# Kernel optimization log

Hardware: AMD Instinct MI355X
Metric: run time of the kernel (lower is better)

## Reference

```python
import jax, jax.numpy as jnp
import numpy as np

HD_DIM = 4096
BUNDLE_SIZE = 128
STRIDE = 128  # bundle_size - overlap, overlap = 0
EPS = 1e-8


def setup_inputs() -> dict:
    key = jax.random.key(0)
    k1, k2 = jax.random.split(key)
    inputs = jax.random.normal(k1, (4, 2048, HD_DIM), dtype=jnp.float32)
    # base vector ~ N(0, 1/sqrt(hd_dim)) as in RandomNormal(stddev=1/sqrt(hd_dim))
    base = jax.random.normal(k2, (HD_DIM,), dtype=jnp.float32) / jnp.sqrt(jnp.float32(HD_DIM))
    # position_weights initialized to decay_rate**i
    pos_w = jnp.power(jnp.float32(0.99), jnp.arange(BUNDLE_SIZE, dtype=jnp.float32))
    return {"inputs": inputs, "bundle_position_base": base, "position_weights": pos_w}


def reference(inputs, bundle_position_base, position_weights):
    B, S, D = inputs.shape
    nb = (S - BUNDLE_SIZE) // STRIDE + 1  # number of bundles

    # Cyclic-shift position vectors: pos[s, d] = base[(d - s) mod D]
    shifts = jnp.arange(BUNDLE_SIZE)
    idx = jnp.mod(jnp.arange(D)[None, :] - shifts[:, None], D)  # [bs, D]
    pos = bundle_position_base[idx]                              # [bs, D]
    w = jax.nn.softmax(position_weights)                         # [bs]
    pos = pos * w[:, None]

    # overlap=0 and S divisible by bundle_size -> bundles tile the sequence
    tok = inputs.reshape(B, nb, BUNDLE_SIZE, D)  # [B, nb, bs, D]

    # circular correlation: real(ifft(fft(tok) * conj(fft(pos))))
    # both operands real -> use rfft/irfft (identical math, half the work)
    tok_f = jnp.fft.rfft(tok, axis=-1)                 # [B, nb, bs, D//2+1]
    pos_f = jnp.conj(jnp.fft.rfft(pos, axis=-1))       # [bs, D//2+1]
    bound = jnp.fft.irfft(tok_f * pos_f[None, None], n=D, axis=-1)  # [B, nb, bs, D]

    bundle = jnp.sum(bound, axis=2)  # [B, nb, D]
    # tf.nn.l2_normalize: x * rsqrt(max(sum(x^2), eps))
    ssq = jnp.sum(bundle * bundle, axis=-1, keepdims=True)
    return (bundle * jax.lax.rsqrt(jnp.maximum(ssq, EPS))).astype(jnp.float32)
```

## Files before the change

kernel.cpp:

```cpp
#include <hip/hip_runtime.h>

#define D 4096
#define DM 4095
#define BS 128
#define NROW 64
#define JC 8

#define ZSTR 520
#define PSTR 616

typedef __attribute__((ext_vector_type(8))) short bf16x8;
typedef __attribute__((ext_vector_type(4))) float f32x4;

__device__ __forceinline__ unsigned short f2bf(float f) {
  union { float f; unsigned int u; } v;
  v.f = f;
  const unsigned int r = v.u + 0x7fffu + ((v.u >> 16) & 1u);
  return (unsigned short)(r >> 16);
}

__global__ __launch_bounds__(256) void zshift_k(const float* __restrict__ tok,
                                                const float* __restrict__ pw,
                                                unsigned short* __restrict__ zb) {
  const int t = threadIdx.x;
  const int mc = blockIdx.x;
  const int row = blockIdx.y;

  __shared__ float wsh[BS];
  __shared__ float red[4];
  __shared__ float4 xsh[128];
  {
    const float v = (t < BS) ? pw[t] : -1e30f;
    float m = v;
#pragma unroll
    for (int o = 32; o > 0; o >>= 1) m = fmaxf(m, __shfl_xor(m, o));
    if ((t & 63) == 0) red[t >> 6] = m;
    __syncthreads();
    m = fmaxf(fmaxf(red[0], red[1]), fmaxf(red[2], red[3]));
    const float e = (t < BS) ? expf(v - m) : 0.f;
    float s = e;
#pragma unroll
    for (int o = 32; o > 0; o >>= 1) s += __shfl_xor(s, o);
    __syncthreads();
    if ((t & 63) == 0) red[t >> 6] = s;
    __syncthreads();
    s = red[0] + red[1] + red[2] + red[3];
    if (t < BS) wsh[t] = e / s;
    __syncthreads();
  }

  const int g = t & 127;
  const int h = t >> 7;
  const int og = (mc << 7) + g;
  const float4* tr = (const float4*)(tok + (size_t)row * (BS * D));

  float4 acc = make_float4(0.f, 0.f, 0.f, 0.f);
#pragma unroll
  for (int qq = 0; qq < 16; ++qq) {
    const int q = (h << 4) + qq;
    const float w0 = wsh[4 * q + 0], w1 = wsh[4 * q + 1];
    const float w2 = wsh[4 * q + 2], w3 = wsh[4 * q + 3];
    const int G = (og + q) & 1023;
    const int G1 = (G + 1) & 1023;
    const size_t r0 = (size_t)(4 * q + 0) << 10;
    const size_t r1 = (size_t)(4 * q + 1) << 10;
    const size_t r2 = (size_t)(4 * q + 2) << 10;
    const size_t r3 = (size_t)(4 * q + 3) << 10;
    const float4 a0 = tr[r0 + G];
    const float4 a1 = tr[r1 + G], b1 = tr[r1 + G1];
    const float4 a2 = tr[r2 + G], b2 = tr[r2 + G1];
    const float4 a3 = tr[r3 + G], b3 = tr[r3 + G1];
    acc.x += w0 * a0.x; acc.y += w0 * a0.y;
    acc.z += w0 * a0.z; acc.w += w0 * a0.w;
    acc.x += w1 * a1.y; acc.y += w1 * a1.z;
    acc.z += w1 * a1.w; acc.w += w1 * b1.x;
    acc.x += w2 * a2.z; acc.y += w2 * a2.w;
    acc.z += w2 * b2.x; acc.w += w2 * b2.y;
    acc.x += w3 * a3.w; acc.y += w3 * b3.x;
    acc.z += w3 * b3.y; acc.w += w3 * b3.z;
  }
  if (h) xsh[g] = acc;
  __syncthreads();
  if (!h) {
    const float4 o = xsh[g];
    ushort4 u;
    u.x = f2bf(acc.x + o.x);
    u.y = f2bf(acc.y + o.y);
    u.z = f2bf(acc.z + o.z);
    u.w = f2bf(acc.w + o.w);
    *(ushort4*)(zb + (size_t)row * D + ((size_t)og << 2)) = u;
  }
}

__global__ __launch_bounds__(256) void corr_k(const unsigned short* __restrict__ zb,
                                              const float* __restrict__ base,
                                              float* __restrict__ braw) {
  __shared__ __align__(16) unsigned short zsh[16 * ZSTR];
  __shared__ __align__(16) unsigned short psh[8 * PSTR];
  const int t = threadIdx.x;
  const int jc = blockIdx.x;
  const int dg = blockIdx.y;
  const int rt = blockIdx.z;
  const int jb = jc << 9;
  const int d0b = dg << 6;

  {
    const int rr = t >> 4;
    const int c0 = (t & 15) << 5;
    const uint4* src =
        (const uint4*)(zb + (size_t)(rt * 16 + rr) * D + jb + c0);
    uint4* dst = (uint4*)(zsh + rr * ZSTR + c0);
    dst[0] = src[0];
    dst[1] = src[1];
    dst[2] = src[2];
    dst[3] = src[3];
  }
  {
    const int c0 = jb - d0b - 64 + 2 * D;
    for (int idx = t; idx < 8 * PSTR; idx += 256) {
      const int r = idx / PSTR;
      const int x = idx - r * PSTR;
      psh[idx] = f2bf(base[(c0 + r + x) & DM]);
    }
  }
  __syncthreads();

  const int lane = t & 63;
  const int w = t >> 6;
  const int dd = lane & 15;
  const int q = lane >> 4;
  const int a0 = 64 + (q << 3) - (w << 4) - dd;
  const int pr = a0 & 7;
  const int px = a0 - pr;
  const unsigned short* pA = psh + pr * PSTR + px;
  const unsigned short* pB = zsh + dd * ZSTR + (q << 3);

  f32x4 acc = {0.f, 0.f, 0.f, 0.f};
#pragma unroll
  for (int ks = 0; ks < 16; ++ks) {
    const bf16x8 af = *(const bf16x8*)(pA + (ks << 5));
    const bf16x8 bf = *(const bf16x8*)(pB + (ks << 5));
    acc = __builtin_amdgcn_mfma_f32_16x16x32_bf16(af, bf, acc, 0, 0, 0);
  }
  const int row = rt * 16 + dd;
  const int d = d0b + (w << 4) + (q << 2);
  float4 o = make_float4(acc[0], acc[1], acc[2], acc[3]);
  *(float4*)(braw + (size_t)(jc * NROW + row) * D + d) = o;
}

__global__ __launch_bounds__(1024) void norm_k(const float* __restrict__ braw,
                                               float* __restrict__ out) {
  const int t = threadIdx.x;
  const int row = blockIdx.x;
  const float4* b4 = (const float4*)braw;
  float4 s = make_float4(0.f, 0.f, 0.f, 0.f);
#pragma unroll
  for (int p = 0; p < JC; ++p) {
    const float4 v = b4[(size_t)(p * NROW + row) * (D / 4) + t];
    s.x += v.x; s.y += v.y; s.z += v.z; s.w += v.w;
  }
  float ssq = s.x * s.x + s.y * s.y + s.z * s.z + s.w * s.w;
#pragma unroll
  for (int o = 32; o > 0; o >>= 1) ssq += __shfl_xor(ssq, o);
  __shared__ float red[16];
  if ((t & 63) == 0) red[t >> 6] = ssq;
  __syncthreads();
  float tot = 0.f;
#pragma unroll
  for (int i = 0; i < 16; ++i) tot += red[i];
  const float sc = rsqrtf(fmaxf(tot, 1e-8f));
  float4 o;
  o.x = s.x * sc; o.y = s.y * sc; o.z = s.z * sc; o.w = s.w * sc;
  ((float4*)out)[(size_t)row * (D / 4) + t] = o;
}

extern "C" void kernel_launch(void* const* d_in, const int* in_sizes, int n_in,
                              void* d_out, int out_size, void* d_ws, size_t ws_size,
                              hipStream_t stream) {
  (void)in_sizes; (void)n_in; (void)out_size; (void)ws_size;
  const float* tok = (const float*)d_in[0];
  const float* base = (const float*)d_in[1];
  const float* pw = (const float*)d_in[2];
  float* out = (float*)d_out;

  unsigned short* zb = (unsigned short*)d_ws;
  float* braw = (float*)(zb + (size_t)NROW * D);

  zshift_k<<<dim3(8, NROW), 256, 0, stream>>>(tok, pw, zb);
  corr_k<<<dim3(JC, 64, 4), 256, 0, stream>>>(zb, base, braw);
  norm_k<<<NROW, 1024, 0, stream>>>(braw, out);
}
```

Baseline: 205.8 us.

## Accumulate all j-chunks inside corr_k with double-buffered LDS, drop partial buffer

corr_k now loops over the 8 j-chunks per block, double-buffering the z and position tiles in LDS and keeping the MFMA accumulator in registers. This removes the per-chunk partial output writes and the 8-way reduction in norm_k. The trade-off is 8x fewer blocks, which cuts parallelism and occupancy, and the staging of each chunk is serialized with compute inside a block.

```diff
diff --git a/kernel.cpp b/kernel.cpp
--- a/kernel.cpp
+++ b/kernel.cpp
@@ -4,7 +4,6 @@
 #define DM 4095
 #define BS 128
 #define NROW 64
-#define JC 8
 
 #define ZSTR 520
 #define PSTR 616
@@ -94,36 +93,35 @@
 
 __global__ __launch_bounds__(256) void corr_k(const unsigned short* __restrict__ zb,
                                               const float* __restrict__ base,
-                                              float* __restrict__ braw) {
-  __shared__ __align__(16) unsigned short zsh[16 * ZSTR];
-  __shared__ __align__(16) unsigned short psh[8 * PSTR];
+                                              float* __restrict__ bundle) {
+  __shared__ __align__(16) unsigned short zsh[2][16 * ZSTR];
+  __shared__ __align__(16) unsigned short psh[2][8 * PSTR];
   const int t = threadIdx.x;
-  const int jc = blockIdx.x;
-  const int dg = blockIdx.y;
-  const int rt = blockIdx.z;
-  const int jb = jc << 9;
+  const int dg = blockIdx.x;
+  const int rt = blockIdx.y;
   const int d0b = dg << 6;
 
-  {
-    const int rr = t >> 4;
-    const int c0 = (t & 15) << 5;
-    const uint4* src =
-        (const uint4*)(zb + (size_t)(rt * 16 + rr) * D + jb + c0);
-    uint4* dst = (uint4*)(zsh + rr * ZSTR + c0);
-    dst[0] = src[0];
-    dst[1] = src[1];
-    dst[2] = src[2];
-    dst[3] = src[3];
+  const int rr = t >> 4;
+  const int c0 = (t & 15) << 5;
+  const uint4* zsrc0 =
+      (const uint4*)(zb + (size_t)(rt * 16 + rr) * D + c0);
+
+#define STAGE(jc, b)                                                        \
+  {                                                                         \
+    const int jb_ = (jc) << 9;                                              \
+    const uint4* src_ = zsrc0 + (jb_ >> 3);                                 \
+    uint4* dst_ = (uint4*)(zsh[b] + rr * ZSTR + c0);                        \
+    dst_[0] = src_[0]; dst_[1] = src_[1];                                   \
+    dst_[2] = src_[2]; dst_[3] = src_[3];                                   \
+    const int c0p_ = jb_ - d0b - 64 + 2 * D;                                \
+    for (int idx = t; idx < 8 * PSTR; idx += 256) {                         \
+      const int r_ = idx / PSTR;                                           \
+      const int x_ = idx - r_ * PSTR;                                      \
+      psh[b][idx] = f2bf(base[(c0p_ + r_ + x_) & DM]);                      \
+    }                                                                       \
   }
-  {
-    const int c0 = jb - d0b - 64 + 2 * D;
-    for (int idx = t; idx < 8 * PSTR; idx += 256) {
-      const int r = idx / PSTR;
-      const int x = idx - r * PSTR;
-      psh[idx] = f2bf(base[(c0 + r + x) & DM]);
-    }
-  }
-  __syncthreads();
+
+  STAGE(0, 0);
 
   const int lane = t & 63;
   const int w = t >> 6;
@@ -132,33 +130,35 @@
   const int a0 = 64 + (q << 3) - (w << 4) - dd;
   const int pr = a0 & 7;
   const int px = a0 - pr;
-  const unsigned short* pA = psh + pr * PSTR + px;
-  const unsigned short* pB = zsh + dd * ZSTR + (q << 3);
+  const int aoff = pr * PSTR + px;
+  const int boff = dd * ZSTR + (q << 3);
 
   f32x4 acc = {0.f, 0.f, 0.f, 0.f};
+#pragma unroll 1
+  for (int jc = 0; jc < 8; ++jc) {
+    __syncthreads();
+    if (jc < 7) STAGE(jc + 1, (jc + 1) & 1);
+    const unsigned short* pA = psh[jc & 1] + aoff;
+    const unsigned short* pB = zsh[jc & 1] + boff;
 #pragma unroll
-  for (int ks = 0; ks < 16; ++ks) {
-    const bf16x8 af = *(const bf16x8*)(pA + (ks << 5));
-    const bf16x8 bf = *(const bf16x8*)(pB + (ks << 5));
-    acc = __builtin_amdgcn_mfma_f32_16x16x32_bf16(af, bf, acc, 0, 0, 0);
+    for (int ks = 0; ks < 16; ++ks) {
+      const bf16x8 af = *(const bf16x8*)(pA + (ks << 5));
+      const bf16x8 bf = *(const bf16x8*)(pB + (ks << 5));
+      acc = __builtin_amdgcn_mfma_f32_16x16x32_bf16(af, bf, acc, 0, 0, 0);
+    }
   }
+#undef STAGE
   const int row = rt * 16 + dd;
   const int d = d0b + (w << 4) + (q << 2);
   float4 o = make_float4(acc[0], acc[1], acc[2], acc[3]);
-  *(float4*)(braw + (size_t)(jc * NROW + row) * D + d) = o;
+  *(float4*)(bundle + (size_t)row * D + d) = o;
 }
 
-__global__ __launch_bounds__(1024) void norm_k(const float* __restrict__ braw,
+__global__ __launch_bounds__(1024) void norm_k(const float* __restrict__ bundle,
                                                float* __restrict__ out) {
   const int t = threadIdx.x;
   const int row = blockIdx.x;
-  const float4* b4 = (const float4*)braw;
-  float4 s = make_float4(0.f, 0.f, 0.f, 0.f);
-#pragma unroll
-  for (int p = 0; p < JC; ++p) {
-    const float4 v = b4[(size_t)(p * NROW + row) * (D / 4) + t];
-    s.x += v.x; s.y += v.y; s.z += v.z; s.w += v.w;
-  }
+  const float4 s = ((const float4*)bundle)[(size_t)row * (D / 4) + t];
   float ssq = s.x * s.x + s.y * s.y + s.z * s.z + s.w * s.w;
 #pragma unroll
   for (int o = 32; o > 0; o >>= 1) ssq += __shfl_xor(ssq, o);
@@ -184,9 +184,9 @@
   float* out = (float*)d_out;
 
   unsigned short* zb = (unsigned short*)d_ws;
-  float* braw = (float*)(zb + (size_t)NROW * D);
+  float* bundle = (float*)(zb + (size_t)NROW * D);
 
   zshift_k<<<dim3(8, NROW), 256, 0, stream>>>(tok, pw, zb);
-  corr_k<<<dim3(JC, 64, 4), 256, 0, stream>>>(zb, base, braw);
-  norm_k<<<NROW, 1024, 0, stream>>>(braw, out);
+  corr_k<<<dim3(64, 4), 256, 0, stream>>>(zb, base, bundle);
+  norm_k<<<NROW, 1024, 0, stream>>>(bundle, out);
 }
```

Result: slower. 211.4 us (+2.7%).
